# Kernel optimization log

Measured on AMD Instinct MI355X. Metric: run time of the kernel, lower is better.

## Reference

```python
import jax, jax.numpy as jnp
import numpy as np

N = 50000
E = 800000
IN_C = 128
HID = 64
HEADS = 4
NEG_SLOPE = 0.2
EPS = 1e-16


def setup_inputs() -> dict:
    key = jax.random.key(0)
    ks = jax.random.split(key, 12)
    x = jax.random.normal(ks[0], (N, IN_C), dtype=jnp.float32)
    edge_index = jax.random.randint(ks[1], (2, E), 0, N, dtype=jnp.int64)
    # layer 1: in -> (HEADS, HID), concat heads
    W1 = jax.random.normal(ks[2], (IN_C, HEADS * HID), dtype=jnp.float32) * (1.0 / np.sqrt(IN_C))
    a_src1 = jax.random.normal(ks[3], (HEADS, HID), dtype=jnp.float32) * 0.1
    a_dst1 = jax.random.normal(ks[4], (HEADS, HID), dtype=jnp.float32) * 0.1
    b1 = jnp.zeros((HEADS * HID,), dtype=jnp.float32)
    # layer 2: HEADS*HID -> (1, HID)
    W2 = jax.random.normal(ks[5], (HEADS * HID, HID), dtype=jnp.float32) * (1.0 / np.sqrt(HEADS * HID))
    a_src2 = jax.random.normal(ks[6], (1, HID), dtype=jnp.float32) * 0.1
    a_dst2 = jax.random.normal(ks[7], (1, HID), dtype=jnp.float32) * 0.1
    b2 = jnp.zeros((HID,), dtype=jnp.float32)
    return {"x": x, "edge_index": edge_index, "W1": W1, "a_src1": a_src1,
            "a_dst1": a_dst1, "b1": b1, "W2": W2, "a_src2": a_src2,
            "a_dst2": a_dst2, "b2": b2}


def _gat_conv(x, src, dst, W, a_src, a_dst, bias, heads, ch):
    n = x.shape[0]
    h = (x @ W).reshape(n, heads, ch)                       # [N,H,C]
    alpha_s = jnp.einsum('nhc,hc->nh', h, a_src)            # [N,H]
    alpha_d = jnp.einsum('nhc,hc->nh', h, a_dst)            # [N,H]
    e = jax.nn.leaky_relu(alpha_s[src] + alpha_d[dst], NEG_SLOPE)  # [E,H]
    # segment softmax over incoming edges of each dst node
    m = jax.ops.segment_max(e, dst, num_segments=n)         # [N,H]
    ex = jnp.exp(e - m[dst])
    denom = jax.ops.segment_sum(ex, dst, num_segments=n)    # [N,H]
    alpha = ex / (denom[dst] + EPS)                         # [E,H]
    msg = h[src] * alpha[:, :, None]                        # [E,H,C]
    out = jax.ops.segment_sum(msg, dst, num_segments=n)     # [N,H,C]
    return out.reshape(n, heads * ch) + bias


def reference(x, edge_index, W1, a_src1, a_dst1, b1, W2, a_src2, a_dst2, b2):
    src = edge_index[0]
    dst = edge_index[1]
    h = _gat_conv(x, src, dst, W1, a_src1, a_dst1, b1, HEADS, HID)
    h = jax.nn.elu(h)
    h = _gat_conv(h, src, dst, W2, a_src2, a_dst2, b2, 1, HID)
    h = jax.nn.elu(h)
    return h  # [N, HID] (output_dim == hidden_channels so no final linear)
```

## Files before the change

kernel.cpp:

```cpp
#include <hip/hip_runtime.h>
#include <math.h>

#define NN 50000
#define EE 800000
#define IN_C 128
#define HID 64
#define HEADS 4
#define SCAN_BLOCKS ((NN + 255) / 256)
#define EBLOCKS ((EE + 255) / 256)

typedef __attribute__((ext_vector_type(8))) short bf16x8;
typedef __attribute__((ext_vector_type(4))) float f32x4;

#if defined(__has_builtin)
#if __has_builtin(__builtin_amdgcn_fdot2_f32_bf16)
#define HAVE_FDOT2_BF16 1
#endif
#endif


__device__ inline unsigned short f2bf(float f) {
    unsigned u = __float_as_uint(f);
    return (unsigned short)((u + 0x7fff + ((u >> 16) & 1)) >> 16);
}
__device__ inline float bf2f(unsigned short s) {
    return __uint_as_float(((unsigned)s) << 16);
}
__device__ inline unsigned prm(unsigned a, unsigned b, unsigned sel) {
    return __builtin_amdgcn_perm(a, b, sel);
}
#ifdef HAVE_FDOT2_BF16
typedef __attribute__((ext_vector_type(2))) __bf16 bf2v;
__device__ inline float fdot2bf(unsigned h, unsigned w, float acc) {
    return __builtin_amdgcn_fdot2_f32_bf16(__builtin_bit_cast(bf2v, h),
                                           __builtin_bit_cast(bf2v, w), acc, false);
}
#else
__device__ inline float fdot2bf(unsigned h, unsigned w, float acc) {
    return acc + bf2f((unsigned short)(h & 0xffff)) * bf2f((unsigned short)(w & 0xffff))
               + bf2f((unsigned short)(h >> 16)) * bf2f((unsigned short)(w >> 16));
}
#endif

__device__ inline int wave_incl_scan(int v, int lane) {
    #pragma unroll
    for (int off = 1; off < 64; off <<= 1) {
        int t = __shfl_up(v, off);
        if (lane >= off) v += t;
    }
    return v;
}

__device__ inline int block256_excl_scan(int v, int tid, int* ws4) {
    int lane = tid & 63, wv = tid >> 6;
    int incl = wave_incl_scan(v, lane);
    if (lane == 63) ws4[wv] = incl;
    __syncthreads();
    if (tid == 0) {
        int run = 0;
        #pragma unroll
        for (int i = 0; i < 4; i++) { int t = ws4[i]; ws4[i] = run; run += t; }
    }
    __syncthreads();
    return incl + ws4[wv] - v;
}


__global__ void front_kernel(const int* __restrict__ ei, int* __restrict__ deg,
                             unsigned short* __restrict__ rank,
                             const float* __restrict__ W1, unsigned short* __restrict__ W1Thi,
                             unsigned short* __restrict__ W1Tlo,
                             const float* __restrict__ W2, unsigned short* __restrict__ W2Thi,
                             unsigned short* __restrict__ W2Tlo) {
    int b = blockIdx.x;
    int tid = threadIdx.x;
    if (b < EBLOCKS) {
        int i = b * 256 + tid;
        if (i < EE) rank[i] = (unsigned short)atomicAdd(&deg[ei[EE + i]], 1);
    } else if (b < EBLOCKS + 128) {
        int idx = (b - EBLOCKS) * 256 + tid;
        int r = idx >> 8, c = idx & 255;
        float v = W1[idx];
        unsigned short h = f2bf(v);
        W1Thi[c * 128 + r] = h;
        W1Tlo[c * 128 + r] = f2bf(v - bf2f(h));
    } else {
        int idx = (b - EBLOCKS - 128) * 256 + tid;
        int r = idx >> 6, c = idx & 63;
        float v = W2[idx];
        unsigned short h = f2bf(v);
        W2Thi[c * 256 + r] = h;
        W2Tlo[c * 256 + r] = f2bf(v - bf2f(h));
    }
}

__global__ void scan_fill_kernel(const int* __restrict__ deg,
                                 unsigned long long* __restrict__ desc,
                                 int* __restrict__ row_ptr) {
    __shared__ int ws4[4];
    __shared__ int sbase;
    int b = blockIdx.x, tid = threadIdx.x;
    int idx = b * 256 + tid;
    int d = (idx < NN) ? deg[idx] : 0;
    int excl = block256_excl_scan(d, tid, ws4);
    if (tid == 255) {
        unsigned total = (unsigned)(excl + d);
        __threadfence();
        atomicExch(&desc[b], (1ULL << 32) | (unsigned long long)total);
    }
    if (tid < 64) {
        int sum = 0;
        int hi = b;
        while (hi > 0) {
            int lo = hi - 64; if (lo < 0) lo = 0;
            int myi = lo + tid;
            unsigned v = 0;
            if (myi < hi) {
                unsigned long long d8;
                do { d8 = atomicAdd(&desc[myi], 0ULL); } while ((d8 >> 32) == 0);
                v = (unsigned)(d8 & 0xffffffffULL);
            }
            #pragma unroll
            for (int off = 32; off; off >>= 1) v += __shfl_down(v, off);
            v = __shfl(v, 0);
            sum += (int)v;
            hi = lo;
        }
        if (tid == 0) sbase = sum;
    }
    __syncthreads();
    int gbase = sbase;
    if (idx < NN) row_ptr[idx] = gbase + excl;
    if (b == gridDim.x - 1 && tid == 255) row_ptr[NN] = gbase + excl + d;
}

__global__ void scatter_kernel(const int* __restrict__ ei, const unsigned short* __restrict__ rank,
                               const int* __restrict__ row_ptr, unsigned short* __restrict__ csr_src) {
    int i = blockIdx.x * blockDim.x + threadIdx.x;
    if (i < EE) {
        int d = ei[EE + i];
        csr_src[row_ptr[d] + (int)rank[i]] = (unsigned short)ei[i];
    }
}

__global__ __launch_bounds__(256) void gemm1_mfma(
        const float* __restrict__ x,
        const unsigned short* __restrict__ Bhi, const unsigned short* __restrict__ Blo,
        const float* __restrict__ a_src, const float* __restrict__ a_dst,
        unsigned short* __restrict__ h1b, float* __restrict__ as1, float* __restrict__ ad1) {
    __shared__ unsigned short Ahi[64][136];
    __shared__ unsigned short Alo[64][136];
    int tid = threadIdx.x;
    int w = tid >> 6, lane = tid & 63;
    int lq = lane >> 4, lr = lane & 15;
    int brow = blockIdx.x * 64;
    {
        int row = tid >> 2;
        int col0 = (tid & 3) * 32;
        int gr = min(brow + row, NN - 1);
        #pragma unroll
        for (int i = 0; i < 32; i += 4) {
            float4 v = *(const float4*)(x + (size_t)gr * 128 + col0 + i);
            unsigned short h0 = f2bf(v.x), h1 = f2bf(v.y), h2 = f2bf(v.z), h3 = f2bf(v.w);
            Ahi[row][col0 + i + 0] = h0; Alo[row][col0 + i + 0] = f2bf(v.x - bf2f(h0));
            Ahi[row][col0 + i + 1] = h1; Alo[row][col0 + i + 1] = f2bf(v.y - bf2f(h1));
            Ahi[row][col0 + i + 2] = h2; Alo[row][col0 + i + 2] = f2bf(v.z - bf2f(h2));
            Ahi[row][col0 + i + 3] = h3; Alo[row][col0 + i + 3] = f2bf(v.w - bf2f(h3));
        }
    }
    __syncthreads();
    f32x4 acc[4][4];
    f32x4 zf = {0.f, 0.f, 0.f, 0.f};
    #pragma unroll
    for (int mi = 0; mi < 4; mi++)
        #pragma unroll
        for (int ni = 0; ni < 4; ni++) acc[mi][ni] = zf;
    #pragma unroll
    for (int q = 0; q < 4; q++) {
        int ko = q * 32 + lq * 8;
        bf16x8 ah[4], al[4];
        #pragma unroll
        for (int mi = 0; mi < 4; mi++) {
            ah[mi] = *(const bf16x8*)(const void*)&Ahi[mi * 16 + lr][ko];
            al[mi] = *(const bf16x8*)(const void*)&Alo[mi * 16 + lr][ko];
        }
        #pragma unroll
        for (int ni = 0; ni < 4; ni++) {
            size_t bo = (size_t)(w * 64 + ni * 16 + lr) * 128 + ko;
            bf16x8 bh = *(const bf16x8*)(const void*)(Bhi + bo);
            bf16x8 bl = *(const bf16x8*)(const void*)(Blo + bo);
            #pragma unroll
            for (int mi = 0; mi < 4; mi++) {
                acc[mi][ni] = __builtin_amdgcn_mfma_f32_16x16x32_bf16(al[mi], bh, acc[mi][ni], 0, 0, 0);
                acc[mi][ni] = __builtin_amdgcn_mfma_f32_16x16x32_bf16(ah[mi], bl, acc[mi][ni], 0, 0, 0);
                acc[mi][ni] = __builtin_amdgcn_mfma_f32_16x16x32_bf16(ah[mi], bh, acc[mi][ni], 0, 0, 0);
            }
        }
    }
    float asv[4], adv[4];
    #pragma unroll
    for (int ni = 0; ni < 4; ni++) {
        asv[ni] = a_src[w * 64 + ni * 16 + lr];
        adv[ni] = a_dst[w * 64 + ni * 16 + lr];
    }
    #pragma unroll
    for (int mi = 0; mi < 4; mi++) {
        f32x4 ps = zf, pd = zf;
        #pragma unroll
        for (int ni = 0; ni < 4; ni++)
            #pragma unroll
            for (int r = 0; r < 4; r++) {
                ps[r] += acc[mi][ni][r] * asv[ni];
                pd[r] += acc[mi][ni][r] * adv[ni];
            }
        #pragma unroll
        for (int m = 1; m < 16; m <<= 1)
            #pragma unroll
            for (int r = 0; r < 4; r++) {
                ps[r] += __shfl_xor(ps[r], m);
                pd[r] += __shfl_xor(pd[r], m);
            }
        #pragma unroll
        for (int r = 0; r < 4; r++) {
            int n = brow + mi * 16 + lq * 4 + r;
            if (lr == 0 && n < NN) { as1[n * 4 + w] = ps[r]; ad1[n * 4 + w] = pd[r]; }
        }
        #pragma unroll
        for (int ni = 0; ni < 4; ni++)
            #pragma unroll
            for (int r = 0; r < 4; r++) {
                int n = brow + mi * 16 + lq * 4 + r;
                if (n < NN)
                    h1b[(size_t)n * 256 + w * 64 + ni * 16 + lr] = f2bf(acc[mi][ni][r]);
            }
    }
}

__global__ __launch_bounds__(256) void gemm2_mfma(
        const unsigned short* __restrict__ Ab,
        const unsigned short* __restrict__ Bhi, const unsigned short* __restrict__ Blo,
        const float* __restrict__ a_src, const float* __restrict__ a_dst,
        unsigned short* __restrict__ g2b, float* __restrict__ as2, float* __restrict__ ad2) {
    int tid = threadIdx.x;
    int w = tid >> 6, lane = tid & 63;
    int lq = lane >> 4, lr = lane & 15;
    int wrow = blockIdx.x * 128 + w * 32;
    f32x4 acc[2][4];
    f32x4 zf = {0.f, 0.f, 0.f, 0.f};
    #pragma unroll
    for (int mi = 0; mi < 2; mi++)
        #pragma unroll
        for (int ni = 0; ni < 4; ni++) acc[mi][ni] = zf;
    int ra = min(wrow + lr, NN - 1);
    int rb = min(wrow + 16 + lr, NN - 1);
    #pragma unroll
    for (int q = 0; q < 8; q++) {
        int ko = q * 32 + lq * 8;
        bf16x8 ah0 = *(const bf16x8*)(const void*)(Ab + (size_t)ra * 256 + ko);
        bf16x8 ah1 = *(const bf16x8*)(const void*)(Ab + (size_t)rb * 256 + ko);
        #pragma unroll
        for (int ni = 0; ni < 4; ni++) {
            size_t bo = (size_t)(ni * 16 + lr) * 256 + ko;
            bf16x8 bh = *(const bf16x8*)(const void*)(Bhi + bo);
            bf16x8 bl = *(const bf16x8*)(const void*)(Blo + bo);
            acc[0][ni] = __builtin_amdgcn_mfma_f32_16x16x32_bf16(ah0, bl, acc[0][ni], 0, 0, 0);
            acc[0][ni] = __builtin_amdgcn_mfma_f32_16x16x32_bf16(ah0, bh, acc[0][ni], 0, 0, 0);
            acc[1][ni] = __builtin_amdgcn_mfma_f32_16x16x32_bf16(ah1, bl, acc[1][ni], 0, 0, 0);
            acc[1][ni] = __builtin_amdgcn_mfma_f32_16x16x32_bf16(ah1, bh, acc[1][ni], 0, 0, 0);
        }
    }
    float asv[4], adv[4];
    #pragma unroll
    for (int ni = 0; ni < 4; ni++) {
        asv[ni] = a_src[ni * 16 + lr];
        adv[ni] = a_dst[ni * 16 + lr];
    }
    #pragma unroll
    for (int mi = 0; mi < 2; mi++) {
        f32x4 ps = zf, pd = zf;
        #pragma unroll
        for (int ni = 0; ni < 4; ni++)
            #pragma unroll
            for (int r = 0; r < 4; r++) {
                ps[r] += acc[mi][ni][r] * asv[ni];
                pd[r] += acc[mi][ni][r] * adv[ni];
            }
        #pragma unroll
        for (int m = 1; m < 16; m <<= 1)
            #pragma unroll
            for (int r = 0; r < 4; r++) {
                ps[r] += __shfl_xor(ps[r], m);
                pd[r] += __shfl_xor(pd[r], m);
            }
        #pragma unroll
        for (int r = 0; r < 4; r++) {
            int n = wrow + mi * 16 + lq * 4 + r;
            if (lr == 0 && n < NN) { as2[n] = ps[r]; ad2[n] = pd[r]; }
        }
        #pragma unroll
        for (int ni = 0; ni < 4; ni++)
            #pragma unroll
            for (int r = 0; r < 4; r++) {
                int n = wrow + mi * 16 + lq * 4 + r;
                if (n < NN)
                    g2b[(size_t)n * 64 + ni * 16 + lr] = f2bf(acc[mi][ni][r]);
            }
    }
}

__global__ __launch_bounds__(256) void agg1_kernel(
        const unsigned short* __restrict__ h1b, const int* __restrict__ row_ptr,
        const unsigned short* __restrict__ csr_src, const float* __restrict__ as,
        const float* __restrict__ ad, const float* __restrict__ b1,
        unsigned short* __restrict__ h2b) {
    __shared__ int            ssrc[4][64];
    __shared__ unsigned short wbf[4][4][64];
    int tid = threadIdx.x;
    int wv = tid >> 6, lane = tid & 63;
    int n = blockIdx.x * 4 + wv;
    if (n >= NN) return;
    int start = row_ptr[n], end = row_ptr[n + 1];
    float4 adv = ((const float4*)ad)[n];
    int whead = lane >> 4;
    float4 acc = make_float4(0.f, 0.f, 0.f, 0.f);
    float d0 = 0.f, d1 = 0.f, d2 = 0.f, d3 = 0.f;
    for (int c0 = start; c0 < end; c0 += 64) {
        int m = min(64, end - c0);
        if (lane < m) {
            int s = (int)csr_src[c0 + lane];
            ssrc[wv][lane] = s;
            float4 asv = ((const float4*)as)[s];
            float e0 = asv.x + adv.x; e0 = e0 > 0.f ? e0 : 0.2f * e0; float x0 = __expf(e0);
            float e1 = asv.y + adv.y; e1 = e1 > 0.f ? e1 : 0.2f * e1; float x1 = __expf(e1);
            float e2 = asv.z + adv.z; e2 = e2 > 0.f ? e2 : 0.2f * e2; float x2 = __expf(e2);
            float e3 = asv.w + adv.w; e3 = e3 > 0.f ? e3 : 0.2f * e3; float x3 = __expf(e3);
            wbf[wv][0][lane] = f2bf(x0);
            wbf[wv][1][lane] = f2bf(x1);
            wbf[wv][2][lane] = f2bf(x2);
            wbf[wv][3][lane] = f2bf(x3);
            d0 += x0; d1 += x1; d2 += x2; d3 += x3;
        }
        int j = 0;
        for (; j + 8 <= m; j += 8) {
            int sj[8]; uint2 hj[8];
            #pragma unroll
            for (int u = 0; u < 8; u++) sj[u] = ssrc[wv][j + u];
            #pragma unroll
            for (int u = 0; u < 8; u++)
                hj[u] = ((const uint2*)h1b)[(size_t)sj[u] * 64 + lane];
            unsigned wp01 = *(const unsigned*)&wbf[wv][whead][j];
            unsigned wp23 = *(const unsigned*)&wbf[wv][whead][j + 2];
            unsigned wp45 = *(const unsigned*)&wbf[wv][whead][j + 4];
            unsigned wp67 = *(const unsigned*)&wbf[wv][whead][j + 6];
            acc.x = fdot2bf(prm(hj[1].x, hj[0].x, 0x05040100), wp01, acc.x);
            acc.y = fdot2bf(prm(hj[1].x, hj[0].x, 0x07060302), wp01, acc.y);
            acc.z = fdot2bf(prm(hj[1].y, hj[0].y, 0x05040100), wp01, acc.z);
            acc.w = fdot2bf(prm(hj[1].y, hj[0].y, 0x07060302), wp01, acc.w);
            acc.x = fdot2bf(prm(hj[3].x, hj[2].x, 0x05040100), wp23, acc.x);
            acc.y = fdot2bf(prm(hj[3].x, hj[2].x, 0x07060302), wp23, acc.y);
            acc.z = fdot2bf(prm(hj[3].y, hj[2].y, 0x05040100), wp23, acc.z);
            acc.w = fdot2bf(prm(hj[3].y, hj[2].y, 0x07060302), wp23, acc.w);
            acc.x = fdot2bf(prm(hj[5].x, hj[4].x, 0x05040100), wp45, acc.x);
            acc.y = fdot2bf(prm(hj[5].x, hj[4].x, 0x07060302), wp45, acc.y);
            acc.z = fdot2bf(prm(hj[5].y, hj[4].y, 0x05040100), wp45, acc.z);
            acc.w = fdot2bf(prm(hj[5].y, hj[4].y, 0x07060302), wp45, acc.w);
            acc.x = fdot2bf(prm(hj[7].x, hj[6].x, 0x05040100), wp67, acc.x);
            acc.y = fdot2bf(prm(hj[7].x, hj[6].x, 0x07060302), wp67, acc.y);
            acc.z = fdot2bf(prm(hj[7].y, hj[6].y, 0x05040100), wp67, acc.z);
            acc.w = fdot2bf(prm(hj[7].y, hj[6].y, 0x07060302), wp67, acc.w);
        }
        for (; j + 2 <= m; j += 2) {
            int s0 = ssrc[wv][j], s1 = ssrc[wv][j + 1];
            uint2 ha = ((const uint2*)h1b)[(size_t)s0 * 64 + lane];
            uint2 hb = ((const uint2*)h1b)[(size_t)s1 * 64 + lane];
            unsigned wp = *(const unsigned*)&wbf[wv][whead][j];
            acc.x = fdot2bf(prm(hb.x, ha.x, 0x05040100), wp, acc.x);
            acc.y = fdot2bf(prm(hb.x, ha.x, 0x07060302), wp, acc.y);
            acc.z = fdot2bf(prm(hb.y, ha.y, 0x05040100), wp, acc.z);
            acc.w = fdot2bf(prm(hb.y, ha.y, 0x07060302), wp, acc.w);
        }
        if (j < m) {
            int s = ssrc[wv][j];
            float w = bf2f(wbf[wv][whead][j]);
            ushort4 hv = ((const ushort4*)h1b)[(size_t)s * 64 + lane];
            acc.x += bf2f(hv.x) * w; acc.y += bf2f(hv.y) * w;
            acc.z += bf2f(hv.z) * w; acc.w += bf2f(hv.w) * w;
        }
    }
    #pragma unroll
    for (int off = 32; off; off >>= 1) {
        d0 += __shfl_down(d0, off); d1 += __shfl_down(d1, off);
        d2 += __shfl_down(d2, off); d3 += __shfl_down(d3, off);
    }
    d0 = __shfl(d0, 0); d1 = __shfl(d1, 0);
    d2 = __shfl(d2, 0); d3 = __shfl(d3, 0);
    float den = whead == 0 ? d0 : whead == 1 ? d1 : whead == 2 ? d2 : d3;
    float inv = 1.f / (den + 1e-16f);
    float4 bv = ((const float4*)b1)[lane];
    float4 r;
    r.x = acc.x * inv + bv.x; r.y = acc.y * inv + bv.y;
    r.z = acc.z * inv + bv.z; r.w = acc.w * inv + bv.w;
    r.x = r.x > 0.f ? r.x : expm1f(r.x);
    r.y = r.y > 0.f ? r.y : expm1f(r.y);
    r.z = r.z > 0.f ? r.z : expm1f(r.z);
    r.w = r.w > 0.f ? r.w : expm1f(r.w);
    ushort4 hv;
    hv.x = f2bf(r.x); hv.y = f2bf(r.y); hv.z = f2bf(r.z); hv.w = f2bf(r.w);
    ((ushort4*)h2b)[(size_t)n * 64 + lane] = hv;
}

__global__ __launch_bounds__(256) void agg2_kernel(
        const unsigned short* __restrict__ g2b, const int* __restrict__ row_ptr,
        const unsigned short* __restrict__ csr_src, const float* __restrict__ as,
        const float* __restrict__ ad, const float* __restrict__ b2,
        float* __restrict__ out) {
    __shared__ int            ssrc[4][64];
    __shared__ unsigned short wbf[4][64];
    int tid = threadIdx.x;
    int wv = tid >> 6, lane = tid & 63;
    int n = blockIdx.x * 4 + wv;
    if (n >= NN) return;
    int start = row_ptr[n], end = row_ptr[n + 1];
    float adv = ad[n];
    float acc = 0.f;
    float den = 0.f;
    for (int c0 = start; c0 < end; c0 += 64) {
        int m = min(64, end - c0);
        if (lane < m) {
            int s = (int)csr_src[c0 + lane];
            ssrc[wv][lane] = s;
            float e = as[s] + adv;
            e = e > 0.f ? e : 0.2f * e;
            float x = __expf(e);
            wbf[wv][lane] = f2bf(x);
            den += x;
        }
        int j = 0;
        for (; j + 8 <= m; j += 8) {
            int sj[8]; unsigned gj[8];
            #pragma unroll
            for (int u = 0; u < 8; u++) sj[u] = ssrc[wv][j + u];
            #pragma unroll
            for (int u = 0; u < 8; u++)
                gj[u] = g2b[(size_t)sj[u] * 64 + lane];
            unsigned wp01 = *(const unsigned*)&wbf[wv][j];
            unsigned wp23 = *(const unsigned*)&wbf[wv][j + 2];
            unsigned wp45 = *(const unsigned*)&wbf[wv][j + 4];
            unsigned wp67 = *(const unsigned*)&wbf[wv][j + 6];
            acc = fdot2bf(prm(gj[1], gj[0], 0x05040100), wp01, acc);
            acc = fdot2bf(prm(gj[3], gj[2], 0x05040100), wp23, acc);
            acc = fdot2bf(prm(gj[5], gj[4], 0x05040100), wp45, acc);
            acc = fdot2bf(prm(gj[7], gj[6], 0x05040100), wp67, acc);
        }
        for (; j + 2 <= m; j += 2) {
            int s0 = ssrc[wv][j], s1 = ssrc[wv][j + 1];
            unsigned g0 = g2b[(size_t)s0 * 64 + lane];
            unsigned g1 = g2b[(size_t)s1 * 64 + lane];
            unsigned wp = *(const unsigned*)&wbf[wv][j];
            acc = fdot2bf(prm(g1, g0, 0x05040100), wp, acc);
        }
        if (j < m) {
            int s = ssrc[wv][j];
            acc += bf2f(g2b[(size_t)s * 64 + lane]) * bf2f(wbf[wv][j]);
        }
    }
    #pragma unroll
    for (int off = 32; off; off >>= 1) den += __shfl_down(den, off);
    den = __shfl(den, 0);
    float inv = 1.f / (den + 1e-16f);
    float r = acc * inv + b2[lane];
    out[(size_t)n * 64 + lane] = r > 0.f ? r : expm1f(r);
}


extern "C" void kernel_launch(void* const* d_in, const int* in_sizes, int n_in,
                              void* d_out, int out_size, void* d_ws, size_t ws_size,
                              hipStream_t stream) {
    const float* x      = (const float*)d_in[0];
    const int*   ei     = (const int*)d_in[1];
    const float* W1     = (const float*)d_in[2];
    const float* a_src1 = (const float*)d_in[3];
    const float* a_dst1 = (const float*)d_in[4];
    const float* b1     = (const float*)d_in[5];
    const float* W2     = (const float*)d_in[6];
    const float* a_src2 = (const float*)d_in[7];
    const float* a_dst2 = (const float*)d_in[8];
    const float* b2     = (const float*)d_in[9];
    float* out = (float*)d_out;

    char* base = (char*)d_ws;
    size_t off = 0;
    auto alloc = [&](size_t bytes) -> void* {
        void* p = base + off;
        off = (off + bytes + 255) & ~(size_t)255;
        return p;
    };
    int*   deg     = (int*)alloc(NN * sizeof(int));
    unsigned long long* desc = (unsigned long long*)alloc(SCAN_BLOCKS * sizeof(unsigned long long));
    unsigned short* rank = (unsigned short*)alloc(EE * sizeof(unsigned short));
    int*   row_ptr = (int*)alloc((NN + 1) * sizeof(int));
    unsigned short* csr_src = (unsigned short*)alloc(EE * sizeof(unsigned short));
    unsigned short* W1Thi = (unsigned short*)alloc(256 * 128 * 2);
    unsigned short* W1Tlo = (unsigned short*)alloc(256 * 128 * 2);
    unsigned short* W2Thi = (unsigned short*)alloc(64 * 256 * 2);
    unsigned short* W2Tlo = (unsigned short*)alloc(64 * 256 * 2);
    unsigned short* h1b   = (unsigned short*)alloc((size_t)NN * 256 * 2);
    float* as1     = (float*)alloc((size_t)NN * 4 * sizeof(float));
    float* ad1     = (float*)alloc((size_t)NN * 4 * sizeof(float));
    unsigned short* h2b   = (unsigned short*)alloc((size_t)NN * 256 * 2);
    unsigned short* g2b   = (unsigned short*)alloc((size_t)NN * 64 * 2);
    float* as2     = (float*)alloc((size_t)NN * sizeof(float));
    float* ad2     = (float*)alloc((size_t)NN * sizeof(float));

    size_t clear_bytes = (size_t)((char*)(desc + SCAN_BLOCKS) - (char*)deg);
    hipMemsetAsync(deg, 0, clear_bytes, stream);

    front_kernel<<<EBLOCKS + 128 + 64, 256, 0, stream>>>(ei, deg, rank, W1, W1Thi, W1Tlo,
                                                         W2, W2Thi, W2Tlo);
    scan_fill_kernel<<<SCAN_BLOCKS, 256, 0, stream>>>(deg, desc, row_ptr);
    scatter_kernel<<<EBLOCKS, 256, 0, stream>>>(ei, rank, row_ptr, csr_src);

    gemm1_mfma<<<(NN + 63) / 64, 256, 0, stream>>>(x, W1Thi, W1Tlo,
                                                   a_src1, a_dst1, h1b, as1, ad1);
    agg1_kernel<<<(NN + 3) / 4, 256, 0, stream>>>(h1b, row_ptr, csr_src, as1, ad1, b1, h2b);
    gemm2_mfma<<<(NN + 127) / 128, 256, 0, stream>>>(h2b, W2Thi, W2Tlo,
                                                     a_src2, a_dst2, g2b, as2, ad2);
    agg2_kernel<<<(NN + 3) / 4, 256, 0, stream>>>(g2b, row_ptr, csr_src, as2, ad2, b2, out);
}
```

Before: 284.2 us.

## Split layer-1 aggregation into weight-normalization pass and feature-sliced aggregation

Replaces the fused layer-1 aggregation with two kernels. The first computes normalized softmax edge weights per head and stores them in bf16. The second splits the 256 feature columns into 8 slices of 32 across separate blocks, so each block gathers a narrower slice of h1 and the working set per pass may fit better in cache. The layer-1 output is now stored slice-major, and gemm2 reads that layout. The gemm1 input conversion also switches to packed bf16 conversion with 32-bit LDS stores. In exchange it adds an extra kernel, a 6.4MB weight buffer, csr_src reads repeated 8 times, and 8x more blocks with cross-lane reductions.

```diff
diff --git a/kernel.cpp b/kernel.cpp
--- a/kernel.cpp
+++ b/kernel.cpp
@@ -16,6 +16,9 @@
 #if __has_builtin(__builtin_amdgcn_fdot2_f32_bf16)
 #define HAVE_FDOT2_BF16 1
 #endif
+#if __has_builtin(__builtin_amdgcn_cvt_pk_bf16_f32)
+#define HAVE_PK_BF16 1
+#endif
 #endif
 
 
@@ -26,6 +29,17 @@
 __device__ inline float bf2f(unsigned short s) {
     return __uint_as_float(((unsigned)s) << 16);
 }
+#ifdef HAVE_PK_BF16
+typedef __attribute__((ext_vector_type(2))) __bf16 bf16x2_t;
+__device__ inline unsigned pk2bf(float a, float b) {
+    bf16x2_t r = __builtin_amdgcn_cvt_pk_bf16_f32(a, b);
+    return __builtin_bit_cast(unsigned, r);
+}
+#else
+__device__ inline unsigned pk2bf(float a, float b) {
+    return (unsigned)f2bf(a) | ((unsigned)f2bf(b) << 16);
+}
+#endif
 __device__ inline unsigned prm(unsigned a, unsigned b, unsigned sel) {
     return __builtin_amdgcn_perm(a, b, sel);
 }
@@ -161,11 +175,16 @@
         #pragma unroll
         for (int i = 0; i < 32; i += 4) {
             float4 v = *(const float4*)(x + (size_t)gr * 128 + col0 + i);
-            unsigned short h0 = f2bf(v.x), h1 = f2bf(v.y), h2 = f2bf(v.z), h3 = f2bf(v.w);
-            Ahi[row][col0 + i + 0] = h0; Alo[row][col0 + i + 0] = f2bf(v.x - bf2f(h0));
-            Ahi[row][col0 + i + 1] = h1; Alo[row][col0 + i + 1] = f2bf(v.y - bf2f(h1));
-            Ahi[row][col0 + i + 2] = h2; Alo[row][col0 + i + 2] = f2bf(v.z - bf2f(h2));
-            Ahi[row][col0 + i + 3] = h3; Alo[row][col0 + i + 3] = f2bf(v.w - bf2f(h3));
+            unsigned h01 = pk2bf(v.x, v.y);
+            unsigned h23 = pk2bf(v.z, v.w);
+            float rx = v.x - __uint_as_float(h01 << 16);
+            float ry = v.y - __uint_as_float(h01 & 0xffff0000u);
+            float rz = v.z - __uint_as_float(h23 << 16);
+            float rw = v.w - __uint_as_float(h23 & 0xffff0000u);
+            *(unsigned*)&Ahi[row][col0 + i]     = h01;
+            *(unsigned*)&Ahi[row][col0 + i + 2] = h23;
+            *(unsigned*)&Alo[row][col0 + i]     = pk2bf(rx, ry);
+            *(unsigned*)&Alo[row][col0 + i + 2] = pk2bf(rz, rw);
         }
     }
     __syncthreads();
@@ -236,8 +255,110 @@
     }
 }
 
+__global__ __launch_bounds__(256) void wnorm_kernel(
+        const int* __restrict__ row_ptr, const unsigned short* __restrict__ csr_src,
+        const float* __restrict__ as, const float* __restrict__ ad,
+        unsigned short* __restrict__ wnorm) {
+    int tid = threadIdx.x;
+    int wv = tid >> 6, lane = tid & 63;
+    int n = blockIdx.x * 4 + wv;
+    if (n >= NN) return;
+    int start = row_ptr[n], end = row_ptr[n + 1];
+    float4 adv = ((const float4*)ad)[n];
+    float d0 = 0.f, d1 = 0.f, d2 = 0.f, d3 = 0.f;
+    for (int i = start + lane; i < end; i += 64) {
+        int s = (int)csr_src[i];
+        float4 a = ((const float4*)as)[s];
+        float e;
+        e = a.x + adv.x; e = e > 0.f ? e : 0.2f * e; d0 += __expf(e);
+        e = a.y + adv.y; e = e > 0.f ? e : 0.2f * e; d1 += __expf(e);
+        e = a.z + adv.z; e = e > 0.f ? e : 0.2f * e; d2 += __expf(e);
+        e = a.w + adv.w; e = e > 0.f ? e : 0.2f * e; d3 += __expf(e);
+    }
+    #pragma unroll
+    for (int off = 32; off; off >>= 1) {
+        d0 += __shfl_down(d0, off); d1 += __shfl_down(d1, off);
+        d2 += __shfl_down(d2, off); d3 += __shfl_down(d3, off);
+    }
+    d0 = __shfl(d0, 0); d1 = __shfl(d1, 0);
+    d2 = __shfl(d2, 0); d3 = __shfl(d3, 0);
+    float i0 = 1.f / (d0 + 1e-16f), i1 = 1.f / (d1 + 1e-16f);
+    float i2 = 1.f / (d2 + 1e-16f), i3 = 1.f / (d3 + 1e-16f);
+    for (int i = start + lane; i < end; i += 64) {
+        int s = (int)csr_src[i];
+        float4 a = ((const float4*)as)[s];
+        float e;
+        e = a.x + adv.x; e = e > 0.f ? e : 0.2f * e;
+        wnorm[(size_t)0 * EE + i] = f2bf(__expf(e) * i0);
+        e = a.y + adv.y; e = e > 0.f ? e : 0.2f * e;
+        wnorm[(size_t)1 * EE + i] = f2bf(__expf(e) * i1);
+        e = a.z + adv.z; e = e > 0.f ? e : 0.2f * e;
+        wnorm[(size_t)2 * EE + i] = f2bf(__expf(e) * i2);
+        e = a.w + adv.w; e = e > 0.f ? e : 0.2f * e;
+        wnorm[(size_t)3 * EE + i] = f2bf(__expf(e) * i3);
+    }
+}
+
+__global__ __launch_bounds__(256) void agg1s_kernel(
+        const unsigned short* __restrict__ h1b, const int* __restrict__ row_ptr,
+        const unsigned short* __restrict__ csr_src, const unsigned short* __restrict__ wnorm,
+        const float* __restrict__ b1, unsigned short* __restrict__ h2s) {
+    __shared__ int            ssrc[4][64];
+    __shared__ unsigned short swt[4][64];
+    int tid = threadIdx.x;
+    int wv = tid >> 6, lane = tid & 63;
+    int sl = blockIdx.x & 7;
+    int n = (blockIdx.x >> 3) * 4 + wv;
+    if (n >= NN) return;
+    const unsigned short* wH = wnorm + (size_t)(sl >> 1) * EE;
+    int start = row_ptr[n], end = row_ptr[n + 1];
+    int e8 = lane >> 2;
+    int q  = lane & 3;
+    float acc[8] = {};
+    for (int c0 = start; c0 < end; c0 += 64) {
+        int m = min(64, end - c0);
+        if (lane < m) {
+            ssrc[wv][lane] = (int)csr_src[c0 + lane];
+            swt[wv][lane]  = wH[c0 + lane];
+        } else {
+            ssrc[wv][lane] = 0;
+            swt[wv][lane]  = 0;
+        }
+        for (int j = 0; j < m; j += 16) {
+            int ee = j + e8;
+            int src = ssrc[wv][ee];
+            float w = bf2f(swt[wv][ee]);
+            uint4 hv = *(const uint4*)(const void*)(h1b + (size_t)src * 256 + sl * 32 + q * 8);
+            acc[0] += __uint_as_float(hv.x << 16) * w;
+            acc[1] += __uint_as_float(hv.x & 0xffff0000u) * w;
+            acc[2] += __uint_as_float(hv.y << 16) * w;
+            acc[3] += __uint_as_float(hv.y & 0xffff0000u) * w;
+            acc[4] += __uint_as_float(hv.z << 16) * w;
+            acc[5] += __uint_as_float(hv.z & 0xffff0000u) * w;
+            acc[6] += __uint_as_float(hv.w << 16) * w;
+            acc[7] += __uint_as_float(hv.w & 0xffff0000u) * w;
+        }
+    }
+    #pragma unroll
+    for (int msk = 4; msk < 64; msk <<= 1)
+        #pragma unroll
+        for (int k = 0; k < 8; k++) acc[k] += __shfl_xor(acc[k], msk);
+    if (lane < 4) {
+        float r[8];
+        #pragma unroll
+        for (int k = 0; k < 8; k++) {
+            float v = acc[k] + b1[sl * 32 + lane * 8 + k];
+            r[k] = v > 0.f ? v : expm1f(v);
+        }
+        uint4 o;
+        o.x = pk2bf(r[0], r[1]); o.y = pk2bf(r[2], r[3]);
+        o.z = pk2bf(r[4], r[5]); o.w = pk2bf(r[6], r[7]);
+        *(uint4*)(void*)(h2s + ((size_t)sl * NN + n) * 32 + lane * 8) = o;
+    }
+}
+
 __global__ __launch_bounds__(256) void gemm2_mfma(
-        const unsigned short* __restrict__ Ab,
+        const unsigned short* __restrict__ h2s,
         const unsigned short* __restrict__ Bhi, const unsigned short* __restrict__ Blo,
         const float* __restrict__ a_src, const float* __restrict__ a_dst,
         unsigned short* __restrict__ g2b, float* __restrict__ as2, float* __restrict__ ad2) {
@@ -255,9 +376,9 @@
     int rb = min(wrow + 16 + lr, NN - 1);
     #pragma unroll
     for (int q = 0; q < 8; q++) {
+        bf16x8 ah0 = *(const bf16x8*)(const void*)(h2s + ((size_t)q * NN + ra) * 32 + lq * 8);
+        bf16x8 ah1 = *(const bf16x8*)(const void*)(h2s + ((size_t)q * NN + rb) * 32 + lq * 8);
         int ko = q * 32 + lq * 8;
-        bf16x8 ah0 = *(const bf16x8*)(const void*)(Ab + (size_t)ra * 256 + ko);
-        bf16x8 ah1 = *(const bf16x8*)(const void*)(Ab + (size_t)rb * 256 + ko);
         #pragma unroll
         for (int ni = 0; ni < 4; ni++) {
             size_t bo = (size_t)(ni * 16 + lr) * 256 + ko;
@@ -306,107 +427,6 @@
                     g2b[(size_t)n * 64 + ni * 16 + lr] = f2bf(acc[mi][ni][r]);
             }
     }
-}
-
-__global__ __launch_bounds__(256) void agg1_kernel(
-        const unsigned short* __restrict__ h1b, const int* __restrict__ row_ptr,
-        const unsigned short* __restrict__ csr_src, const float* __restrict__ as,
-        const float* __restrict__ ad, const float* __restrict__ b1,
-        unsigned short* __restrict__ h2b) {
-    __shared__ int            ssrc[4][64];
-    __shared__ unsigned short wbf[4][4][64];
-    int tid = threadIdx.x;
-    int wv = tid >> 6, lane = tid & 63;
-    int n = blockIdx.x * 4 + wv;
-    if (n >= NN) return;
-    int start = row_ptr[n], end = row_ptr[n + 1];
-    float4 adv = ((const float4*)ad)[n];
-    int whead = lane >> 4;
-    float4 acc = make_float4(0.f, 0.f, 0.f, 0.f);
-    float d0 = 0.f, d1 = 0.f, d2 = 0.f, d3 = 0.f;
-    for (int c0 = start; c0 < end; c0 += 64) {
-        int m = min(64, end - c0);
-        if (lane < m) {
-            int s = (int)csr_src[c0 + lane];
-            ssrc[wv][lane] = s;
-            float4 asv = ((const float4*)as)[s];
-            float e0 = asv.x + adv.x; e0 = e0 > 0.f ? e0 : 0.2f * e0; float x0 = __expf(e0);
-            float e1 = asv.y + adv.y; e1 = e1 > 0.f ? e1 : 0.2f * e1; float x1 = __expf(e1);
-            float e2 = asv.z + adv.z; e2 = e2 > 0.f ? e2 : 0.2f * e2; float x2 = __expf(e2);
-            float e3 = asv.w + adv.w; e3 = e3 > 0.f ? e3 : 0.2f * e3; float x3 = __expf(e3);
-            wbf[wv][0][lane] = f2bf(x0);
-            wbf[wv][1][lane] = f2bf(x1);
-            wbf[wv][2][lane] = f2bf(x2);
-            wbf[wv][3][lane] = f2bf(x3);
-            d0 += x0; d1 += x1; d2 += x2; d3 += x3;
-        }
-        int j = 0;
-        for (; j + 8 <= m; j += 8) {
-            int sj[8]; uint2 hj[8];
-            #pragma unroll
-            for (int u = 0; u < 8; u++) sj[u] = ssrc[wv][j + u];
-            #pragma unroll
-            for (int u = 0; u < 8; u++)
-                hj[u] = ((const uint2*)h1b)[(size_t)sj[u] * 64 + lane];
-            unsigned wp01 = *(const unsigned*)&wbf[wv][whead][j];
-            unsigned wp23 = *(const unsigned*)&wbf[wv][whead][j + 2];
-            unsigned wp45 = *(const unsigned*)&wbf[wv][whead][j + 4];
-            unsigned wp67 = *(const unsigned*)&wbf[wv][whead][j + 6];
-            acc.x = fdot2bf(prm(hj[1].x, hj[0].x, 0x05040100), wp01, acc.x);
-            acc.y = fdot2bf(prm(hj[1].x, hj[0].x, 0x07060302), wp01, acc.y);
-            acc.z = fdot2bf(prm(hj[1].y, hj[0].y, 0x05040100), wp01, acc.z);
-            acc.w = fdot2bf(prm(hj[1].y, hj[0].y, 0x07060302), wp01, acc.w);
-            acc.x = fdot2bf(prm(hj[3].x, hj[2].x, 0x05040100), wp23, acc.x);
-            acc.y = fdot2bf(prm(hj[3].x, hj[2].x, 0x07060302), wp23, acc.y);
-            acc.z = fdot2bf(prm(hj[3].y, hj[2].y, 0x05040100), wp23, acc.z);
-            acc.w = fdot2bf(prm(hj[3].y, hj[2].y, 0x07060302), wp23, acc.w);
-            acc.x = fdot2bf(prm(hj[5].x, hj[4].x, 0x05040100), wp45, acc.x);
-            acc.y = fdot2bf(prm(hj[5].x, hj[4].x, 0x07060302), wp45, acc.y);
-            acc.z = fdot2bf(prm(hj[5].y, hj[4].y, 0x05040100), wp45, acc.z);
-            acc.w = fdot2bf(prm(hj[5].y, hj[4].y, 0x07060302), wp45, acc.w);
-            acc.x = fdot2bf(prm(hj[7].x, hj[6].x, 0x05040100), wp67, acc.x);
-            acc.y = fdot2bf(prm(hj[7].x, hj[6].x, 0x07060302), wp67, acc.y);
-            acc.z = fdot2bf(prm(hj[7].y, hj[6].y, 0x05040100), wp67, acc.z);
-            acc.w = fdot2bf(prm(hj[7].y, hj[6].y, 0x07060302), wp67, acc.w);
-        }
-        for (; j + 2 <= m; j += 2) {
-            int s0 = ssrc[wv][j], s1 = ssrc[wv][j + 1];
-            uint2 ha = ((const uint2*)h1b)[(size_t)s0 * 64 + lane];
-            uint2 hb = ((const uint2*)h1b)[(size_t)s1 * 64 + lane];
-            unsigned wp = *(const unsigned*)&wbf[wv][whead][j];
-            acc.x = fdot2bf(prm(hb.x, ha.x, 0x05040100), wp, acc.x);
-            acc.y = fdot2bf(prm(hb.x, ha.x, 0x07060302), wp, acc.y);
-            acc.z = fdot2bf(prm(hb.y, ha.y, 0x05040100), wp, acc.z);
-            acc.w = fdot2bf(prm(hb.y, ha.y, 0x07060302), wp, acc.w);
-        }
-        if (j < m) {
-            int s = ssrc[wv][j];
-            float w = bf2f(wbf[wv][whead][j]);
-            ushort4 hv = ((const ushort4*)h1b)[(size_t)s * 64 + lane];
-            acc.x += bf2f(hv.x) * w; acc.y += bf2f(hv.y) * w;
-            acc.z += bf2f(hv.z) * w; acc.w += bf2f(hv.w) * w;
-        }
-    }
-    #pragma unroll
-    for (int off = 32; off; off >>= 1) {
-        d0 += __shfl_down(d0, off); d1 += __shfl_down(d1, off);
-        d2 += __shfl_down(d2, off); d3 += __shfl_down(d3, off);
-    }
-    d0 = __shfl(d0, 0); d1 = __shfl(d1, 0);
-    d2 = __shfl(d2, 0); d3 = __shfl(d3, 0);
-    float den = whead == 0 ? d0 : whead == 1 ? d1 : whead == 2 ? d2 : d3;
-    float inv = 1.f / (den + 1e-16f);
-    float4 bv = ((const float4*)b1)[lane];
-    float4 r;
-    r.x = acc.x * inv + bv.x; r.y = acc.y * inv + bv.y;
-    r.z = acc.z * inv + bv.z; r.w = acc.w * inv + bv.w;
-    r.x = r.x > 0.f ? r.x : expm1f(r.x);
-    r.y = r.y > 0.f ? r.y : expm1f(r.y);
-    r.z = r.z > 0.f ? r.z : expm1f(r.z);
-    r.w = r.w > 0.f ? r.w : expm1f(r.w);
-    ushort4 hv;
-    hv.x = f2bf(r.x); hv.y = f2bf(r.y); hv.z = f2bf(r.z); hv.w = f2bf(r.w);
-    ((ushort4*)h2b)[(size_t)n * 64 + lane] = hv;
 }
 
 __global__ __launch_bounds__(256) void agg2_kernel(
@@ -500,6 +520,7 @@
     unsigned short* rank = (unsigned short*)alloc(EE * sizeof(unsigned short));
     int*   row_ptr = (int*)alloc((NN + 1) * sizeof(int));
     unsigned short* csr_src = (unsigned short*)alloc(EE * sizeof(unsigned short));
+    unsigned short* wnorm  = (unsigned short*)alloc((size_t)4 * EE * sizeof(unsigned short));
     unsigned short* W1Thi = (unsigned short*)alloc(256 * 128 * 2);
     unsigned short* W1Tlo = (unsigned short*)alloc(256 * 128 * 2);
     unsigned short* W2Thi = (unsigned short*)alloc(64 * 256 * 2);
@@ -507,7 +528,7 @@
     unsigned short* h1b   = (unsigned short*)alloc((size_t)NN * 256 * 2);
     float* as1     = (float*)alloc((size_t)NN * 4 * sizeof(float));
     float* ad1     = (float*)alloc((size_t)NN * 4 * sizeof(float));
-    unsigned short* h2b   = (unsigned short*)alloc((size_t)NN * 256 * 2);
+    unsigned short* h2s   = (unsigned short*)alloc((size_t)NN * 256 * 2);
     unsigned short* g2b   = (unsigned short*)alloc((size_t)NN * 64 * 2);
     float* as2     = (float*)alloc((size_t)NN * sizeof(float));
     float* ad2     = (float*)alloc((size_t)NN * sizeof(float));
@@ -522,8 +543,10 @@
 
     gemm1_mfma<<<(NN + 63) / 64, 256, 0, stream>>>(x, W1Thi, W1Tlo,
                                                    a_src1, a_dst1, h1b, as1, ad1);
-    agg1_kernel<<<(NN + 3) / 4, 256, 0, stream>>>(h1b, row_ptr, csr_src, as1, ad1, b1, h2b);
-    gemm2_mfma<<<(NN + 127) / 128, 256, 0, stream>>>(h2b, W2Thi, W2Tlo,
+    wnorm_kernel<<<(NN + 3) / 4, 256, 0, stream>>>(row_ptr, csr_src, as1, ad1, wnorm);
+    agg1s_kernel<<<((NN + 3) / 4) * 8, 256, 0, stream>>>(h1b, row_ptr, csr_src, wnorm,
+                                                         b1, h2s);
+    gemm2_mfma<<<(NN + 127) / 128, 256, 0, stream>>>(h2s, W2Thi, W2Tlo,
                                                      a_src2, a_dst2, g2b, as2, ad2);
     agg2_kernel<<<(NN + 3) / 4, 256, 0, stream>>>(g2b, row_ptr, csr_src, as2, ad2, b2, out);
 }
```

Result: slower. 493.1 us (+73.5%).

## Fuse CSR build into one cooperative kernel with grid syncs

Applied to the files above, without the earlier changes.

Replaces the memset, front, decoupled-lookback scan and scatter kernels with a single cooperative kernel of 1024 blocks. Inside it, grid.sync separates zeroing, degree counting, a two-level block scan and the scatter. This removes several launches and the memset. It also switches the x-to-bf16 hi/lo split in gemm1 to packed conversion with 32-bit LDS stores. In exchange it adds five grid-wide barriers and depends on all 1024 blocks being co-resident.

```diff
diff --git a/kernel.cpp b/kernel.cpp
--- a/kernel.cpp
+++ b/kernel.cpp
@@ -1,13 +1,16 @@
 #include <hip/hip_runtime.h>
+#include <hip/hip_cooperative_groups.h>
 #include <math.h>
+
+namespace cg = cooperative_groups;
 
 #define NN 50000
 #define EE 800000
 #define IN_C 128
 #define HID 64
 #define HEADS 4
-#define SCAN_BLOCKS ((NN + 255) / 256)
-#define EBLOCKS ((EE + 255) / 256)
+#define CSRB 1024
+#define CHUNK ((NN + CSRB - 1) / CSRB)
 
 typedef __attribute__((ext_vector_type(8))) short bf16x8;
 typedef __attribute__((ext_vector_type(4))) float f32x4;
@@ -16,6 +19,9 @@
 #if __has_builtin(__builtin_amdgcn_fdot2_f32_bf16)
 #define HAVE_FDOT2_BF16 1
 #endif
+#if __has_builtin(__builtin_amdgcn_cvt_pk_bf16_f32)
+#define HAVE_PK_BF16 1
+#endif
 #endif
 
 
@@ -26,6 +32,17 @@
 __device__ inline float bf2f(unsigned short s) {
     return __uint_as_float(((unsigned)s) << 16);
 }
+#ifdef HAVE_PK_BF16
+typedef __attribute__((ext_vector_type(2))) __bf16 bf16x2_t;
+__device__ inline unsigned pk2bf(float a, float b) {
+    bf16x2_t r = __builtin_amdgcn_cvt_pk_bf16_f32(a, b);
+    return __builtin_bit_cast(unsigned, r);
+}
+#else
+__device__ inline unsigned pk2bf(float a, float b) {
+    return (unsigned)f2bf(a) | ((unsigned)f2bf(b) << 16);
+}
+#endif
 __device__ inline unsigned prm(unsigned a, unsigned b, unsigned sel) {
     return __builtin_amdgcn_perm(a, b, sel);
 }
@@ -66,78 +83,77 @@
 }
 
 
-__global__ void front_kernel(const int* __restrict__ ei, int* __restrict__ deg,
-                             unsigned short* __restrict__ rank,
-                             const float* __restrict__ W1, unsigned short* __restrict__ W1Thi,
-                             unsigned short* __restrict__ W1Tlo,
-                             const float* __restrict__ W2, unsigned short* __restrict__ W2Thi,
-                             unsigned short* __restrict__ W2Tlo) {
-    int b = blockIdx.x;
-    int tid = threadIdx.x;
-    if (b < EBLOCKS) {
-        int i = b * 256 + tid;
-        if (i < EE) rank[i] = (unsigned short)atomicAdd(&deg[ei[EE + i]], 1);
-    } else if (b < EBLOCKS + 128) {
-        int idx = (b - EBLOCKS) * 256 + tid;
+__global__ void __launch_bounds__(256) csr_kernel(
+        const int* __restrict__ ei, int* __restrict__ deg,
+        unsigned short* __restrict__ rank, int* __restrict__ row_ptr,
+        unsigned short* __restrict__ csr_src, int* __restrict__ bsum, int* __restrict__ boff,
+        const float* __restrict__ W1, unsigned short* __restrict__ W1Thi,
+        unsigned short* __restrict__ W1Tlo,
+        const float* __restrict__ W2, unsigned short* __restrict__ W2Thi,
+        unsigned short* __restrict__ W2Tlo) {
+    cg::grid_group grid = cg::this_grid();
+    __shared__ int ws4[4];
+    int tid = threadIdx.x, b = blockIdx.x;
+    int gt = b * 256 + tid, gs = gridDim.x * 256;
+
+    for (int i = gt; i < NN; i += gs) deg[i] = 0;
+    for (int idx = gt; idx < 128 * 256; idx += gs) {
         int r = idx >> 8, c = idx & 255;
         float v = W1[idx];
         unsigned short h = f2bf(v);
         W1Thi[c * 128 + r] = h;
         W1Tlo[c * 128 + r] = f2bf(v - bf2f(h));
-    } else {
-        int idx = (b - EBLOCKS - 128) * 256 + tid;
+    }
+    for (int idx = gt; idx < 256 * 64; idx += gs) {
         int r = idx >> 6, c = idx & 63;
         float v = W2[idx];
         unsigned short h = f2bf(v);
         W2Thi[c * 256 + r] = h;
         W2Tlo[c * 256 + r] = f2bf(v - bf2f(h));
     }
-}
-
-__global__ void scan_fill_kernel(const int* __restrict__ deg,
-                                 unsigned long long* __restrict__ desc,
-                                 int* __restrict__ row_ptr) {
-    __shared__ int ws4[4];
-    __shared__ int sbase;
-    int b = blockIdx.x, tid = threadIdx.x;
-    int idx = b * 256 + tid;
-    int d = (idx < NN) ? deg[idx] : 0;
-    int excl = block256_excl_scan(d, tid, ws4);
-    if (tid == 255) {
-        unsigned total = (unsigned)(excl + d);
-        __threadfence();
-        atomicExch(&desc[b], (1ULL << 32) | (unsigned long long)total);
-    }
-    if (tid < 64) {
-        int sum = 0;
-        int hi = b;
-        while (hi > 0) {
-            int lo = hi - 64; if (lo < 0) lo = 0;
-            int myi = lo + tid;
-            unsigned v = 0;
-            if (myi < hi) {
-                unsigned long long d8;
-                do { d8 = atomicAdd(&desc[myi], 0ULL); } while ((d8 >> 32) == 0);
-                v = (unsigned)(d8 & 0xffffffffULL);
-            }
-            #pragma unroll
-            for (int off = 32; off; off >>= 1) v += __shfl_down(v, off);
-            v = __shfl(v, 0);
-            sum += (int)v;
-            hi = lo;
-        }
-        if (tid == 0) sbase = sum;
-    }
-    __syncthreads();
-    int gbase = sbase;
-    if (idx < NN) row_ptr[idx] = gbase + excl;
-    if (b == gridDim.x - 1 && tid == 255) row_ptr[NN] = gbase + excl + d;
-}
-
-__global__ void scatter_kernel(const int* __restrict__ ei, const unsigned short* __restrict__ rank,
-                               const int* __restrict__ row_ptr, unsigned short* __restrict__ csr_src) {
-    int i = blockIdx.x * blockDim.x + threadIdx.x;
-    if (i < EE) {
+    grid.sync();
+
+    for (int i = gt; i < EE; i += gs)
+        rank[i] = (unsigned short)atomicAdd(&deg[ei[EE + i]], 1);
+    grid.sync();
+
+    {
+        int base = b * CHUNK;
+        int v = 0;
+        for (int j = tid; j < CHUNK; j += 256) {
+            int idx = base + j;
+            if (idx < NN) v += deg[idx];
+        }
+        int lane = tid & 63, wv = tid >> 6;
+        #pragma unroll
+        for (int off = 32; off; off >>= 1) v += __shfl_down(v, off);
+        if (lane == 0) ws4[wv] = v;
+        __syncthreads();
+        if (tid == 0) bsum[b] = ws4[0] + ws4[1] + ws4[2] + ws4[3];
+    }
+    grid.sync();
+
+    if (b == 0) {
+        int s4[4]; int loc = 0;
+        #pragma unroll
+        for (int k = 0; k < 4; k++) { s4[k] = bsum[tid * 4 + k]; loc += s4[k]; }
+        int excl = block256_excl_scan(loc, tid, ws4);
+        #pragma unroll
+        for (int k = 0; k < 4; k++) { boff[tid * 4 + k] = excl; excl += s4[k]; }
+    }
+    grid.sync();
+
+    {
+        int base = b * CHUNK;
+        int idx = base + tid;
+        int d = (tid < CHUNK && idx < NN) ? deg[idx] : 0;
+        int excl = block256_excl_scan(d, tid, ws4) + boff[b];
+        if (tid < CHUNK && idx < NN) row_ptr[idx] = excl;
+        if (tid <= CHUNK && idx == NN) row_ptr[NN] = excl;
+    }
+    grid.sync();
+
+    for (int i = gt; i < EE; i += gs) {
         int d = ei[EE + i];
         csr_src[row_ptr[d] + (int)rank[i]] = (unsigned short)ei[i];
     }
@@ -161,11 +177,16 @@
         #pragma unroll
         for (int i = 0; i < 32; i += 4) {
             float4 v = *(const float4*)(x + (size_t)gr * 128 + col0 + i);
-            unsigned short h0 = f2bf(v.x), h1 = f2bf(v.y), h2 = f2bf(v.z), h3 = f2bf(v.w);
-            Ahi[row][col0 + i + 0] = h0; Alo[row][col0 + i + 0] = f2bf(v.x - bf2f(h0));
-            Ahi[row][col0 + i + 1] = h1; Alo[row][col0 + i + 1] = f2bf(v.y - bf2f(h1));
-            Ahi[row][col0 + i + 2] = h2; Alo[row][col0 + i + 2] = f2bf(v.z - bf2f(h2));
-            Ahi[row][col0 + i + 3] = h3; Alo[row][col0 + i + 3] = f2bf(v.w - bf2f(h3));
+            unsigned h01 = pk2bf(v.x, v.y);
+            unsigned h23 = pk2bf(v.z, v.w);
+            float rx = v.x - __uint_as_float(h01 << 16);
+            float ry = v.y - __uint_as_float(h01 & 0xffff0000u);
+            float rz = v.z - __uint_as_float(h23 << 16);
+            float rw = v.w - __uint_as_float(h23 & 0xffff0000u);
+            *(unsigned*)&Ahi[row][col0 + i]     = h01;
+            *(unsigned*)&Ahi[row][col0 + i + 2] = h23;
+            *(unsigned*)&Alo[row][col0 + i]     = pk2bf(rx, ry);
+            *(unsigned*)&Alo[row][col0 + i + 2] = pk2bf(rz, rw);
         }
     }
     __syncthreads();
@@ -476,8 +497,8 @@
 extern "C" void kernel_launch(void* const* d_in, const int* in_sizes, int n_in,
                               void* d_out, int out_size, void* d_ws, size_t ws_size,
                               hipStream_t stream) {
+    const int*   ei     = (const int*)d_in[1];
     const float* x      = (const float*)d_in[0];
-    const int*   ei     = (const int*)d_in[1];
     const float* W1     = (const float*)d_in[2];
     const float* a_src1 = (const float*)d_in[3];
     const float* a_dst1 = (const float*)d_in[4];
@@ -496,7 +517,8 @@
         return p;
     };
     int*   deg     = (int*)alloc(NN * sizeof(int));
-    unsigned long long* desc = (unsigned long long*)alloc(SCAN_BLOCKS * sizeof(unsigned long long));
+    int*   bsum    = (int*)alloc(CSRB * sizeof(int));
+    int*   boff    = (int*)alloc(CSRB * sizeof(int));
     unsigned short* rank = (unsigned short*)alloc(EE * sizeof(unsigned short));
     int*   row_ptr = (int*)alloc((NN + 1) * sizeof(int));
     unsigned short* csr_src = (unsigned short*)alloc(EE * sizeof(unsigned short));
@@ -512,13 +534,12 @@
     float* as2     = (float*)alloc((size_t)NN * sizeof(float));
     float* ad2     = (float*)alloc((size_t)NN * sizeof(float));
 
-    size_t clear_bytes = (size_t)((char*)(desc + SCAN_BLOCKS) - (char*)deg);
-    hipMemsetAsync(deg, 0, clear_bytes, stream);
-
-    front_kernel<<<EBLOCKS + 128 + 64, 256, 0, stream>>>(ei, deg, rank, W1, W1Thi, W1Tlo,
-                                                         W2, W2Thi, W2Tlo);
-    scan_fill_kernel<<<SCAN_BLOCKS, 256, 0, stream>>>(deg, desc, row_ptr);
-    scatter_kernel<<<EBLOCKS, 256, 0, stream>>>(ei, rank, row_ptr, csr_src);
+    void* args[] = { (void*)&ei, (void*)&deg, (void*)&rank, (void*)&row_ptr,
+                     (void*)&csr_src, (void*)&bsum, (void*)&boff,
+                     (void*)&W1, (void*)&W1Thi, (void*)&W1Tlo,
+                     (void*)&W2, (void*)&W2Thi, (void*)&W2Tlo };
+    hipLaunchCooperativeKernel((const void*)csr_kernel, dim3(CSRB), dim3(256),
+                               args, 0, stream);
 
     gemm1_mfma<<<(NN + 63) / 64, 256, 0, stream>>>(x, W1Thi, W1Tlo,
                                                    a_src1, a_dst1, h1b, as1, ad1);
```

Measured after the change: 781.4 us. +174.9%, slower.
